# Performance work log

Measured on AMD Instinct MI355X. Metric: run time of the kernel, lower is better.

## Reference

```python
import jax, jax.numpy as jnp
import numpy as np

B, L = 1024, 64          # sentences, tokens per sentence
V, E = 100000, 300       # vocab, embedding dim
RH, M, NC = 50, 50, 3    # rnn_hidden, mem_dim, num_class
N = B * L                # total tree nodes


def setup_inputs() -> dict:
    key = jax.random.key(0)
    ks = jax.random.split(key, 24)
    rn = lambda k, s, sc=0.05: jax.random.normal(k, s, dtype=jnp.float32) * sc
    # balanced binary dependency tree per sentence: parent(i) = (i-1)//2
    loc = np.arange(L)
    par_loc = np.where(loc == 0, -1, (loc - 1) // 2)
    parent = np.where(par_loc[None, :] < 0, -1,
                      par_loc[None, :] + np.arange(B)[:, None] * L).reshape(-1)
    depth = np.tile(np.floor(np.log2(loc + 1)).astype(np.int64), B)
    tm = np.zeros(L, np.float32); tm[1:4] = 1.0  # 3 aspect-target tokens/sentence
    return {
        "embed_ids": jax.random.randint(ks[0], (B, L), 0, V),
        "parent": jnp.asarray(parent),
        "depth": jnp.asarray(depth),
        "target_mask": jnp.asarray(np.tile(tm, B)),
        "num_levels": 7,
        "embed_table": rn(ks[1], (V, E), 1.0),
        "W_ih_f": rn(ks[2], (4 * RH, E)), "W_hh_f": rn(ks[3], (4 * RH, RH)),
        "b_f": rn(ks[4], (4 * RH,)),
        "W_ih_b": rn(ks[5], (4 * RH, E)), "W_hh_b": rn(ks[6], (4 * RH, RH)),
        "b_b": rn(ks[7], (4 * RH,)),
        "W_iou": rn(ks[8], (3 * M, 2 * RH)),
        "U_iou_w": rn(ks[9], (3 * M, M)), "U_iou_b": rn(ks[10], (3 * M,)),
        "b_iou": jnp.zeros((3 * M,), jnp.float32),
        "U_f_w": rn(ks[11], (M, M)), "U_f_b": rn(ks[12], (M,)),
        "H_w": rn(ks[13], (M, 2 * RH)), "H_b": rn(ks[14], (M,)),
        "C_w": rn(ks[15], (NC, M)), "C_b": rn(ks[16], (NC,)),
    }


def _lstm(x, W_ih, W_hh, b, reverse):
    # x: (B, L, E) -> (B, L, H); PyTorch gate order i, f, g, o
    xg = jnp.einsum('ble,ge->blg', x, W_ih) + b
    H = W_hh.shape[1]
    def step(carry, xt):
        h, c = carry
        g = xt + h @ W_hh.T
        i, f, gg, o = jnp.split(g, 4, axis=-1)
        c = jax.nn.sigmoid(f) * c + jax.nn.sigmoid(i) * jnp.tanh(gg)
        h = jax.nn.sigmoid(o) * jnp.tanh(c)
        return (h, c), h
    z = jnp.zeros((x.shape[0], H), x.dtype)
    _, hs = jax.lax.scan(step, (z, z), jnp.swapaxes(xg, 0, 1), reverse=reverse)
    return jnp.swapaxes(hs, 0, 1)


def reference(embed_ids, parent, depth, target_mask, num_levels, embed_table,
              W_ih_f, W_hh_f, b_f, W_ih_b, W_hh_b, b_b,
              W_iou, U_iou_w, U_iou_b, b_iou, U_f_w, U_f_b,
              H_w, H_b, C_w, C_b):
    # --- BiLSTM encoder (dropout = identity at inference) ---
    emb = embed_table[embed_ids]                       # (B,L,E) gather
    hf = _lstm(emb, W_ih_f, W_hh_f, b_f, False)
    hb = _lstm(emb, W_ih_b, W_hh_b, b_b, True)
    x = jnp.concatenate([hf, hb], -1).reshape(N, 2 * RH)
    # --- ChildSum TreeLSTM, topological (deepest level first) ---
    iou0 = x @ W_iou.T                                 # (N, 3M)
    h_init = x @ H_w.T + H_b                           # (N, M)
    parent_safe = jnp.where(parent >= 0, parent, N)    # roots -> dummy slot N
    counts = jnp.zeros(N + 1, jnp.int32).at[parent_safe].add(1)
    has_children = (counts[:N] > 0)[:, None]
    h_fin = h_init
    c_fin = jnp.zeros((N, M), jnp.float32)
    h_sum = jnp.zeros((N + 1, M), jnp.float32)         # sum of child h
    fc_sum = jnp.zeros((N + 1, M), jnp.float32)        # sum of f * child c
    for lvl in range(num_levels - 1, -1, -1):
        m = (depth == lvl)[:, None]
        # reduce: leaves never get U_iou bias (no mailbox in DGL)
        iou = iou0 + jnp.where(has_children, h_sum[:N] @ U_iou_w.T + U_iou_b, 0.0) + b_iou
        i, o, u = jnp.split(iou, 3, axis=-1)
        c_new = jax.nn.sigmoid(i) * jnp.tanh(u) + fc_sum[:N]
        h_new = h_init + jax.nn.sigmoid(o) * jnp.tanh(c_new)
        h_fin = jnp.where(m, h_new, h_fin)
        c_fin = jnp.where(m, c_new, c_fin)
        # scatter messages from this level's nodes to their parents
        f = jax.nn.sigmoid(h_new @ U_f_w.T + U_f_b)
        h_sum = h_sum.at[parent_safe].add(jnp.where(m, h_new, 0.0))
        fc_sum = fc_sum.at[parent_safe].add(jnp.where(m, f * c_new, 0.0))
    # --- masked mean pool over target tokens per sentence ---
    tm = target_mask.reshape(B, L)
    pooled = (h_fin.reshape(B, L, M) * tm[:, :, None]).sum(1) / tm.sum(1, keepdims=True)
    logits = pooled @ C_w.T + C_b
    return logits, pooled
```

## Files before the change

### kernel.cpp

```cpp
#include <hip/hip_runtime.h>


typedef __attribute__((ext_vector_type(8))) short bf16x8;
typedef __attribute__((ext_vector_type(4))) float f32x4;

__device__ __forceinline__ float fsig2(float x) {
    float e = __builtin_amdgcn_exp2f(-1.4426950408889634f * x);
    return __builtin_amdgcn_rcpf(1.0f + e);
}
__device__ __forceinline__ float ftanh2(float x) {
    float e = __builtin_amdgcn_exp2f(2.8853900817779268f * x);
    return 1.0f - 2.0f * __builtin_amdgcn_rcpf(1.0f + e);
}

__device__ __forceinline__ unsigned short rne_bf16(float f) {
    unsigned u = __builtin_bit_cast(unsigned, f);
    unsigned r = u + 0x7fffu + ((u >> 16) & 1u);
    return (unsigned short)(r >> 16);
}
__device__ __forceinline__ void split2(float f, unsigned short& h, unsigned short& l) {
    h = rne_bf16(f);
    float fh = __builtin_bit_cast(float, ((unsigned)h) << 16);
    float r = f - fh;
    l = rne_bf16(r);
}

__device__ __forceinline__ void async_lds16(const void* g, void* l) {
    __builtin_amdgcn_global_load_lds(
        (const __attribute__((address_space(1))) unsigned int*)g,
        (__attribute__((address_space(3))) unsigned int*)l, 16, 0, 0);
}

__device__ __forceinline__ bf16x8 pack8(const unsigned short* h) {
    bf16x8 v;
    #pragma unroll
    for (int e = 0; e < 8; ++e) v[e] = (short)h[e];
    return v;
}

__device__ __forceinline__ void conv_item(int q, const float* __restrict__ B1,
                                          const float* __restrict__ B2,
                                          int split, int K, int Rreal, int BN,
                                          unsigned short* __restrict__ out) {
    int n  = q % BN;
    int kq = (q / BN) & 3;
    int c  = q / (BN * 4);
    const float* row = (n < split) ? (B1 + (size_t)n * K) : (B2 + (size_t)(n - split) * K);
    unsigned short h[8], l[8];
    #pragma unroll
    for (int e = 0; e < 8; ++e) {
        int k = c * 32 + kq * 8 + e;
        float v = (n < Rreal && k < K) ? row[k] : 0.0f;
        split2(v, h[e], l[e]);
    }
    size_t hb = ((((size_t)c * 2 + 0) * 4 + kq) * BN + n) * 8;
    size_t lb = ((((size_t)c * 2 + 1) * 4 + kq) * BN + n) * 8;
    *(ushort4*)&out[hb]     = make_ushort4(h[0], h[1], h[2], h[3]);
    *(ushort4*)&out[hb + 4] = make_ushort4(h[4], h[5], h[6], h[7]);
    *(ushort4*)&out[lb]     = make_ushort4(l[0], l[1], l[2], l[3]);
    *(ushort4*)&out[lb + 4] = make_ushort4(l[4], l[5], l[6], l[7]);
}

constexpr int WHC_DIR = 2 * 2 * 4 * 208 * 8;

__global__ void conv_fused(const float* __restrict__ Wihf, const float* __restrict__ Wihb,
                           const float* __restrict__ Wiou, const float* __restrict__ Hw,
                           const float* __restrict__ Whhf, const float* __restrict__ Whhb,
                           unsigned short* __restrict__ B1c,
                           unsigned short* __restrict__ B3c,
                           unsigned short* __restrict__ Whc) {
    int q = blockIdx.x * 256 + threadIdx.x;
    if (q < 17920) {
        conv_item(q, Wihf, Wihb, 200, 300, 400, 448, B1c);
    } else if (q < 22016) {
        conv_item(q - 17920, Wiou, Hw, 150, 100, 200, 256, B3c);
    } else if (q < 23680) {
        conv_item(q - 22016, Whhf, Whhf, 200, 50, 200, 208, Whc);
    } else if (q < 25344) {
        conv_item(q - 23680, Whhb, Whhb, 200, 50, 200, 208, Whc + WHC_DIR);
    }
}

template<int BN, int KCH, int KREAL, int NCOLS, bool GATHER>
__global__ __launch_bounds__(256)
void gemm_db(const float* __restrict__ A, const int* __restrict__ ids,
             const unsigned short* __restrict__ Bc,
             const float* __restrict__ bias1, const float* __restrict__ bias2,
             int split, float* __restrict__ C) {
    static_assert(KREAL % 8 == 4, "tail fixup assumes KREAL%8==4");
    static_assert(KCH % 2 == 0, "paired bodies");
    constexpr int NTW = BN / 64;
    constexpr int CHB = 64 * BN;
    constexpr int DMA_PT = BN / 32;
    __shared__ __align__(16) unsigned short As[2][2 * 4 * 64 * 8];
    __shared__ __align__(16) unsigned short Bt[2][CHB];

    const int tid = threadIdx.x;
    const int m0 = blockIdx.x * 64;
    const int w = tid >> 6, lane = tid & 63;
    const int r16 = lane & 15, quad = lane >> 4;
    const int wn = w * (BN / 4);

    const int mA = tid & 63, kqA = tid >> 6;
    const float* arow = GATHER ? (A + (size_t)ids[m0 + mA] * KREAL)
                               : (A + (size_t)(m0 + mA) * KREAL);

    auto stageB = [&](int c, int slot) {
        int cc = (c < KCH) ? c : (KCH - 1);
        const unsigned short* src = Bc + (size_t)cc * CHB + tid * 8;
        unsigned short* dst = &Bt[slot][tid * 8];
        #pragma unroll
        for (int i = 0; i < DMA_PT; ++i)
            async_lds16(src + (size_t)i * 2048, dst + i * 2048);
    };
    auto issueA = [&](int c, float4& p, float4& q) {
        int cc = (c < KCH) ? c : (KCH - 1);
        int k0 = cc * 32 + kqA * 8;
        const float* src = arow + ((k0 <= KREAL - 8) ? k0 : (KREAL - 8));
        p = *(const float4*)src;
        q = *(const float4*)(src + 4);
    };
    auto asWrite = [&](int c, float4 p, float4 q) {
        float ar[8];
        int k0 = c * 32 + kqA * 8;
        if (k0 <= KREAL - 8) {
            ar[0]=p.x; ar[1]=p.y; ar[2]=p.z; ar[3]=p.w;
            ar[4]=q.x; ar[5]=q.y; ar[6]=q.z; ar[7]=q.w;
        } else {
            ar[0] = (k0 + 0 < KREAL) ? q.x : 0.0f;
            ar[1] = (k0 + 1 < KREAL) ? q.y : 0.0f;
            ar[2] = (k0 + 2 < KREAL) ? q.z : 0.0f;
            ar[3] = (k0 + 3 < KREAL) ? q.w : 0.0f;
            ar[4] = 0.0f; ar[5] = 0.0f; ar[6] = 0.0f; ar[7] = 0.0f;
        }
        unsigned short h[8], l[8];
        #pragma unroll
        for (int e = 0; e < 8; ++e) split2(ar[e], h[e], l[e]);
        *(bf16x8*)&As[c & 1][((0 * 4 + kqA) * 64 + mA) * 8] = pack8(h);
        *(bf16x8*)&As[c & 1][((1 * 4 + kqA) * 64 + mA) * 8] = pack8(l);
    };

    f32x4 acc[4][NTW] = {};

    auto body = [&](int c, float4& wrP, float4& wrQ, float4& ldP, float4& ldQ) {
        stageB(c + 1, (c + 1) & 1);
        __builtin_amdgcn_sched_barrier(0);
        issueA(c + 2, ldP, ldQ);
        __builtin_amdgcn_sched_barrier(0);
        asWrite(c + 1, wrP, wrQ);
        bf16x8 af[2][4];
        #pragma unroll
        for (int i = 0; i < 4; ++i) {
            af[0][i] = *(const bf16x8*)&As[c & 1][((0 * 4 + quad) * 64 + i * 16 + r16) * 8];
            af[1][i] = *(const bf16x8*)&As[c & 1][((1 * 4 + quad) * 64 + i * 16 + r16) * 8];
        }
        #pragma unroll
        for (int t = 0; t < NTW; ++t) {
            bf16x8 bh = *(const bf16x8*)&Bt[c & 1][((0 * 4 + quad) * BN + wn + t * 16 + r16) * 8];
            bf16x8 bl = *(const bf16x8*)&Bt[c & 1][((1 * 4 + quad) * BN + wn + t * 16 + r16) * 8];
            #pragma unroll
            for (int i = 0; i < 4; ++i) {
                acc[i][t] = __builtin_amdgcn_mfma_f32_16x16x32_bf16(af[0][i], bh, acc[i][t], 0, 0, 0);
                acc[i][t] = __builtin_amdgcn_mfma_f32_16x16x32_bf16(af[1][i], bh, acc[i][t], 0, 0, 0);
                acc[i][t] = __builtin_amdgcn_mfma_f32_16x16x32_bf16(af[0][i], bl, acc[i][t], 0, 0, 0);
            }
        }
        asm volatile("s_waitcnt lgkmcnt(0) vmcnt(2)" ::: "memory");
        __builtin_amdgcn_sched_barrier(0);
        __builtin_amdgcn_s_barrier();
        __builtin_amdgcn_sched_barrier(0);
    };

    float4 pA, qA, pB, qB;
    stageB(0, 0);
    __builtin_amdgcn_sched_barrier(0);
    issueA(0, pA, qA);
    issueA(1, pB, qB);
    __syncthreads();
    asWrite(0, pA, qA);
    __syncthreads();

    #pragma unroll 1
    for (int c2 = 0; c2 < KCH / 2; ++c2) {
        body(2 * c2,     pB, qB, pA, qA);
        body(2 * c2 + 1, pA, qA, pB, qB);
    }

    #pragma unroll
    for (int t = 0; t < NTW; ++t) {
        int ncol = wn + t * 16 + r16;
        if (ncol < NCOLS) {
            float bv = (ncol < split) ? bias1[ncol] : bias2[ncol - split];
            #pragma unroll
            for (int i = 0; i < 4; ++i)
                #pragma unroll
                for (int r = 0; r < 4; ++r) {
                    int mrow = m0 + i * 16 + quad * 4 + r;
                    C[(size_t)mrow * NCOLS + ncol] = acc[i][t][r] + bv;
                }
        }
    }
}

__global__ __launch_bounds__(256)
void lstm_mfma(const float* __restrict__ xg, const unsigned short* __restrict__ Whc,
               float* __restrict__ x) {
    const int bi = blockIdx.x;
    const int dir = bi & 1;
    const int b0 = (bi >> 1) * 8;
    const int tid = threadIdx.x;
    const int w = tid >> 6, lane = tid & 63;
    const int r16 = lane & 15, quad = lane >> 4;

    __shared__ __align__(16) unsigned short Ah[8 * 16 * 8];
    __shared__ __align__(16) unsigned short Al[8 * 16 * 8];
    __shared__ __align__(16) float G[208 * 20];
    __shared__ __align__(16) float Xs[3][8][268];

    const int n0 = (w == 0) ? 0 : (w == 1) ? 4 : (w == 2) ? 7 : 10;
    const int nc = (w == 0) ? 4 : 3;

    const unsigned short* Wd = Whc + (size_t)dir * WHC_DIR;
    bf16x8 bfr[4][2][2];
    #pragma unroll
    for (int t = 0; t < 4; ++t) {
        int col = (n0 + ((t < nc) ? t : 0)) * 16 + r16;
        #pragma unroll
        for (int c = 0; c < 2; ++c)
            #pragma unroll
            for (int h = 0; h < 2; ++h)
                bfr[t][c][h] = *(const bf16x8*)&Wd[((((size_t)c * 2 + h) * 4 + quad) * 208 + col) * 8];
    }

    for (int q = tid; q < 512; q += 256) {
        ((unsigned*)Ah)[q] = 0u;
        ((unsigned*)Al)[q] = 0u;
    }

    int ss[2], ms[2];
    bool act[2];
    #pragma unroll
    for (int j = 0; j < 2; ++j) {
        int q = w * 100 + lane + 64 * j;
        ss[j] = q & 7;
        ms[j] = q >> 3;
        act[j] = (lane + 64 * j) < 100;
    }
    float c_reg[2] = {0.0f, 0.0f};

    #pragma unroll
    for (int p = 0; p < 2; ++p) {
        int idx0 = dir ? (63 - p) : p;
        #pragma unroll
        for (int i = 0; i < 2; ++i) {
            int s = w * 2 + i;
            const float* src = xg + ((size_t)(b0 + s) * 64 + idx0) * 400 + dir * 200 + lane * 4;
            async_lds16(src, &Xs[p][s][lane * 4]);
        }
    }
    __syncthreads();

    for (int step = 0; step < 64; ++step) {
        const int buf = step % 3;
        const int idx = dir ? (63 - step) : step;
        {
            int stepn = step + 2; if (stepn > 63) stepn = 63;
            const int slot = (step + 2) % 3;
            const int idxn = dir ? (63 - stepn) : stepn;
            #pragma unroll
            for (int i = 0; i < 2; ++i) {
                int s = w * 2 + i;
                const float* src = xg + ((size_t)(b0 + s) * 64 + idxn) * 400 + dir * 200 + lane * 4;
                async_lds16(src, &Xs[slot][s][lane * 4]);
            }
            __builtin_amdgcn_sched_barrier(0);
        }
        bf16x8 ah[2], al[2];
        #pragma unroll
        for (int c = 0; c < 2; ++c) {
            ah[c] = *(const bf16x8*)&Ah[((c * 4 + quad) * 16 + r16) * 8];
            al[c] = *(const bf16x8*)&Al[((c * 4 + quad) * 16 + r16) * 8];
        }
        f32x4 acc[4] = {};
        #pragma unroll
        for (int t = 0; t < 4; ++t) {
            if (t < nc) {
                #pragma unroll
                for (int c = 0; c < 2; ++c) {
                    acc[t] = __builtin_amdgcn_mfma_f32_16x16x32_bf16(ah[c], bfr[t][c][0], acc[t], 0, 0, 0);
                    acc[t] = __builtin_amdgcn_mfma_f32_16x16x32_bf16(al[c], bfr[t][c][0], acc[t], 0, 0, 0);
                    acc[t] = __builtin_amdgcn_mfma_f32_16x16x32_bf16(ah[c], bfr[t][c][1], acc[t], 0, 0, 0);
                }
            }
        }
        #pragma unroll
        for (int t = 0; t < 4; ++t) {
            if (t < nc) {
                int col = (n0 + t) * 16 + r16;
                *(f32x4*)&G[col * 20 + quad * 4] = acc[t];
            }
        }
        asm volatile("s_waitcnt lgkmcnt(0) vmcnt(8)" ::: "memory");
        __builtin_amdgcn_sched_barrier(0);
        __builtin_amdgcn_s_barrier();
        __builtin_amdgcn_sched_barrier(0);
        #pragma unroll
        for (int j = 0; j < 2; ++j) {
            if (act[j]) {
                int s = ss[j], m = ms[j];
                float gi = G[m * 20 + s]         + Xs[buf][s][m];
                float gf = G[(m + 50) * 20 + s]  + Xs[buf][s][m + 50];
                float gg = G[(m + 100) * 20 + s] + Xs[buf][s][m + 100];
                float go = G[(m + 150) * 20 + s] + Xs[buf][s][m + 150];
                c_reg[j] = fsig2(gf) * c_reg[j] + fsig2(gi) * ftanh2(gg);
                float h = fsig2(go) * ftanh2(c_reg[j]);
                unsigned short hh, hl;
                split2(h, hh, hl);
                Ah[(m >> 3) * 128 + s * 8 + (m & 7)] = hh;
                Al[(m >> 3) * 128 + s * 8 + (m & 7)] = hl;
                x[((size_t)(b0 + s) * 64 + idx) * 100 + dir * 50 + m] = h;
            }
        }
        asm volatile("s_waitcnt lgkmcnt(0)" ::: "memory");
        __builtin_amdgcn_sched_barrier(0);
        __builtin_amdgcn_s_barrier();
        __builtin_amdgcn_sched_barrier(0);
    }
}

__global__ __launch_bounds__(256)
void tree_kernel(const float* __restrict__ C2,
                 const float* __restrict__ Uw, const float* __restrict__ Ub,
                 const float* __restrict__ Fw, const float* __restrict__ Fb,
                 const float* __restrict__ tmask,
                 const float* __restrict__ Cw, const float* __restrict__ Cb,
                 float* __restrict__ out) {
    const int tid = threadIdx.x;
    const int w = tid >> 6, lane = tid & 63;
    const int s = blockIdx.x * 4 + w;

    __shared__ __align__(16) float Us[150][52];
    __shared__ __align__(16) float Fs[50][52];
    __shared__ __align__(16) float HS[4][32][52];
    __shared__ __align__(16) float FC[4][32][52];
    __shared__ __align__(16) float HV[4][64];
    __shared__ __align__(16) float TMS[4][64];

    for (int q = tid; q < 7500; q += 256) Us[q / 50][q % 50] = Uw[q];
    for (int q = tid; q < 2500; q += 256) Fs[q / 50][q % 50] = Fw[q];
    for (int q = tid; q < 4 * 32 * 52; q += 256) {
        int ww = q / (32 * 52), r = q - ww * (32 * 52);
        HS[ww][r / 52][r % 52] = 0.0f;
        FC[ww][r / 52][r % 52] = 0.0f;
    }
    TMS[w][lane] = tmask[(size_t)s * 64 + lane];
    __syncthreads();

    const bool act = lane < 50;
    const int m = act ? lane : 49;
    const float ub0 = Ub[m], ub1 = Ub[50 + m], ub2 = Ub[100 + m];
    const float fb = Fb[m];
    const float* c2s = C2 + (size_t)s * 64 * 200;

    float pr = 0.0f;
    float pc0, pc1, pc2, pc3;
    {
        const float* nb = c2s + 63 * 200;
        pc0 = nb[m]; pc1 = nb[50 + m]; pc2 = nb[100 + m]; pc3 = nb[150 + m];
    }

    for (int l = 6; l >= 0; --l) {
        const int lo = (1 << l) - 1;
        const int hi = min((1 << (l + 1)) - 2, 63);
        for (int loc = lo; loc <= hi; ++loc) {
            const int nxt = (loc < hi) ? (loc + 1) : ((l > 0) ? ((1 << (l - 1)) - 1) : loc);
            float nc0, nc1, nc2, nc3;
            {
                const float* nb = c2s + (size_t)nxt * 200;
                nc0 = nb[m]; nc1 = nb[50 + m]; nc2 = nb[100 + m]; nc3 = nb[150 + m];
            }
            const bool hasch = (loc <= 31);
            float mi = 0.0f, mo = 0.0f, mu = 0.0f, fcv = 0.0f;
            if (hasch) {
                const float* hs = &HS[w][loc][0];
                const float* u0 = &Us[m][0];
                const float* u1 = &Us[50 + m][0];
                const float* u2 = &Us[100 + m][0];
                float i0=0,i1=0,i2=0,i3=0, o0=0,o1=0,o2=0,o3=0, g0=0,g1=0,g2=0,g3=0;
                #pragma unroll
                for (int j = 0; j < 12; ++j) {
                    float4 h4 = *(const float4*)&hs[j * 4];
                    float4 a4 = *(const float4*)&u0[j * 4];
                    float4 b4 = *(const float4*)&u1[j * 4];
                    float4 c4 = *(const float4*)&u2[j * 4];
                    i0 += a4.x*h4.x; i1 += a4.y*h4.y; i2 += a4.z*h4.z; i3 += a4.w*h4.w;
                    o0 += b4.x*h4.x; o1 += b4.y*h4.y; o2 += b4.z*h4.z; o3 += b4.w*h4.w;
                    g0 += c4.x*h4.x; g1 += c4.y*h4.y; g2 += c4.z*h4.z; g3 += c4.w*h4.w;
                }
                float h48 = hs[48], h49 = hs[49];
                mi = ub0 + (i0 + i1) + (i2 + i3) + u0[48]*h48 + u0[49]*h49;
                mo = ub1 + (o0 + o1) + (o2 + o3) + u1[48]*h48 + u1[49]*h49;
                mu = ub2 + (g0 + g1) + (g2 + g3) + u2[48]*h48 + u2[49]*h49;
                fcv = FC[w][loc][m];
            }
            float ig = pc0 + mi, og = pc1 + mo, ug = pc2 + mu;
            float cn = fsig2(ig) * ftanh2(ug) + fcv;
            float hn = pc3 + fsig2(og) * ftanh2(cn);
            pr += TMS[w][loc] * hn;
            if (act) HV[w][lane] = hn;
            {
                const float* hv = &HV[w][0];
                const float* f0 = &Fs[m][0];
                float a0 = 0, a1 = 0, a2 = 0, a3 = 0;
                #pragma unroll
                for (int j = 0; j < 12; ++j) {
                    float4 h4 = *(const float4*)&hv[j * 4];
                    float4 f4 = *(const float4*)&f0[j * 4];
                    a0 += f4.x*h4.x; a1 += f4.y*h4.y; a2 += f4.z*h4.z; a3 += f4.w*h4.w;
                }
                float facc = fb + (a0 + a1) + (a2 + a3) + f0[48]*hv[48] + f0[49]*hv[49];
                if (act && loc > 0) {
                    int p = (loc - 1) >> 1;
                    float fm = fsig2(facc) * cn;
                    HS[w][p][lane] += hn;
                    FC[w][p][lane] += fm;
                }
            }
            pc0 = nc0; pc1 = nc1; pc2 = nc2; pc3 = nc3;
        }
    }

    float ws = 0.0f;
    #pragma unroll
    for (int j = 0; j < 16; ++j) {
        float4 t4 = *(const float4*)&TMS[w][j * 4];
        ws += (t4.x + t4.y) + (t4.z + t4.w);
    }
    float p = pr / ws;
    if (act) {
        out[3072 + (size_t)s * 50 + lane] = p;
        HV[w][lane] = p;
    }
    if (lane < 3) {
        float acc = Cb[lane];
        const float* crow = Cw + lane * 50;
        for (int k = 0; k < 50; ++k) acc += crow[k] * HV[w][k];
        out[(size_t)s * 3 + lane] = acc;
    }
}

extern "C" void kernel_launch(void* const* d_in, const int* in_sizes, int n_in,
                              void* d_out, int out_size, void* d_ws, size_t ws_size,
                              hipStream_t stream) {
    (void)in_sizes; (void)n_in; (void)out_size; (void)ws_size;
    const int*   ids   = (const int*)d_in[0];
    const float* tmask = (const float*)d_in[3];
    const float* table = (const float*)d_in[5];
    const float* Wihf  = (const float*)d_in[6];
    const float* Whhf  = (const float*)d_in[7];
    const float* bf    = (const float*)d_in[8];
    const float* Wihb  = (const float*)d_in[9];
    const float* Whhb  = (const float*)d_in[10];
    const float* bb    = (const float*)d_in[11];
    const float* Wiou  = (const float*)d_in[12];
    const float* Uiouw = (const float*)d_in[13];
    const float* Uioub = (const float*)d_in[14];
    const float* biou  = (const float*)d_in[15];
    const float* Ufw   = (const float*)d_in[16];
    const float* Ufb   = (const float*)d_in[17];
    const float* Hw    = (const float*)d_in[18];
    const float* Hb    = (const float*)d_in[19];
    const float* Cw    = (const float*)d_in[20];
    const float* Cb    = (const float*)d_in[21];
    float* out = (float*)d_out;

    float* wsf = (float*)d_ws;
    float* xg = wsf;
    float* x  = wsf + (size_t)65536 * 400;
    float* C2 = wsf;
    unsigned short* B1c = (unsigned short*)(wsf + 32768000);
    unsigned short* B3c = (unsigned short*)(wsf + 32911360);
    unsigned short* Whc = (unsigned short*)(wsf + 32944128);

    conv_fused<<<99, 256, 0, stream>>>(Wihf, Wihb, Wiou, Hw, Whhf, Whhb,
                                       B1c, B3c, Whc);
    gemm_db<448, 10, 300, 400, true><<<1024, 256, 0, stream>>>(
        table, ids, B1c, bf, bb, 200, xg);
    lstm_mfma<<<256, 256, 0, stream>>>(xg, Whc, x);
    gemm_db<256, 4, 100, 200, false><<<1024, 256, 0, stream>>>(
        x, nullptr, B3c, biou, Hb, 150, C2);
    tree_kernel<<<256, 256, 0, stream>>>(
        C2, Uiouw, Uioub, Ufw, Ufb, tmask, Cw, Cb, out);
}
```

Baseline: 462.2 us.

## Single-buffer B tile in LDS by hoisting B fragments into registers

The GEMM kernel now keeps a single LDS buffer for the B tile instead of two. It first loads all B fragments for the chunk into registers, then synchronizes and issues the async load of the next chunk into the same buffer. Launch bounds ask for two blocks per CU. The aim is to halve B's LDS footprint so occupancy can rise, at the cost of more registers and an extra barrier per iteration, which exposes the B load latency before the MFMAs.

```diff
diff --git a/kernel.cpp b/kernel.cpp
--- a/kernel.cpp
+++ b/kernel.cpp
@@ -82,18 +82,18 @@
 }
 
 template<int BN, int KCH, int KREAL, int NCOLS, bool GATHER>
-__global__ __launch_bounds__(256)
-void gemm_db(const float* __restrict__ A, const int* __restrict__ ids,
-             const unsigned short* __restrict__ Bc,
-             const float* __restrict__ bias1, const float* __restrict__ bias2,
-             int split, float* __restrict__ C) {
+__global__ __launch_bounds__(256, 2)
+void gemm_hoist(const float* __restrict__ A, const int* __restrict__ ids,
+                const unsigned short* __restrict__ Bc,
+                const float* __restrict__ bias1, const float* __restrict__ bias2,
+                int split, float* __restrict__ C) {
     static_assert(KREAL % 8 == 4, "tail fixup assumes KREAL%8==4");
     static_assert(KCH % 2 == 0, "paired bodies");
     constexpr int NTW = BN / 64;
     constexpr int CHB = 64 * BN;
     constexpr int DMA_PT = BN / 32;
     __shared__ __align__(16) unsigned short As[2][2 * 4 * 64 * 8];
-    __shared__ __align__(16) unsigned short Bt[2][CHB];
+    __shared__ __align__(16) unsigned short Bt[CHB];
 
     const int tid = threadIdx.x;
     const int m0 = blockIdx.x * 64;
@@ -105,10 +105,10 @@
     const float* arow = GATHER ? (A + (size_t)ids[m0 + mA] * KREAL)
                                : (A + (size_t)(m0 + mA) * KREAL);
 
-    auto stageB = [&](int c, int slot) {
+    auto stageB = [&](int c) {
         int cc = (c < KCH) ? c : (KCH - 1);
         const unsigned short* src = Bc + (size_t)cc * CHB + tid * 8;
-        unsigned short* dst = &Bt[slot][tid * 8];
+        unsigned short* dst = &Bt[tid * 8];
         #pragma unroll
         for (int i = 0; i < DMA_PT; ++i)
             async_lds16(src + (size_t)i * 2048, dst + i * 2048);
@@ -143,7 +143,17 @@
     f32x4 acc[4][NTW] = {};
 
     auto body = [&](int c, float4& wrP, float4& wrQ, float4& ldP, float4& ldQ) {
-        stageB(c + 1, (c + 1) & 1);
+        bf16x8 bh[NTW], bl[NTW];
+        #pragma unroll
+        for (int t = 0; t < NTW; ++t) {
+            bh[t] = *(const bf16x8*)&Bt[((0 * 4 + quad) * BN + wn + t * 16 + r16) * 8];
+            bl[t] = *(const bf16x8*)&Bt[((1 * 4 + quad) * BN + wn + t * 16 + r16) * 8];
+        }
+        asm volatile("s_waitcnt lgkmcnt(0)" ::: "memory");
+        __builtin_amdgcn_sched_barrier(0);
+        __builtin_amdgcn_s_barrier();
+        __builtin_amdgcn_sched_barrier(0);
+        stageB(c + 1);
         __builtin_amdgcn_sched_barrier(0);
         issueA(c + 2, ldP, ldQ);
         __builtin_amdgcn_sched_barrier(0);
@@ -156,13 +166,11 @@
         }
         #pragma unroll
         for (int t = 0; t < NTW; ++t) {
-            bf16x8 bh = *(const bf16x8*)&Bt[c & 1][((0 * 4 + quad) * BN + wn + t * 16 + r16) * 8];
-            bf16x8 bl = *(const bf16x8*)&Bt[c & 1][((1 * 4 + quad) * BN + wn + t * 16 + r16) * 8];
             #pragma unroll
             for (int i = 0; i < 4; ++i) {
-                acc[i][t] = __builtin_amdgcn_mfma_f32_16x16x32_bf16(af[0][i], bh, acc[i][t], 0, 0, 0);
-                acc[i][t] = __builtin_amdgcn_mfma_f32_16x16x32_bf16(af[1][i], bh, acc[i][t], 0, 0, 0);
-                acc[i][t] = __builtin_amdgcn_mfma_f32_16x16x32_bf16(af[0][i], bl, acc[i][t], 0, 0, 0);
+                acc[i][t] = __builtin_amdgcn_mfma_f32_16x16x32_bf16(af[0][i], bh[t], acc[i][t], 0, 0, 0);
+                acc[i][t] = __builtin_amdgcn_mfma_f32_16x16x32_bf16(af[1][i], bh[t], acc[i][t], 0, 0, 0);
+                acc[i][t] = __builtin_amdgcn_mfma_f32_16x16x32_bf16(af[0][i], bl[t], acc[i][t], 0, 0, 0);
             }
         }
         asm volatile("s_waitcnt lgkmcnt(0) vmcnt(2)" ::: "memory");
@@ -172,7 +180,7 @@
     };
 
     float4 pA, qA, pB, qB;
-    stageB(0, 0);
+    stageB(0);
     __builtin_amdgcn_sched_barrier(0);
     issueA(0, pA, qA);
     issueA(1, pB, qB);
@@ -484,10 +492,10 @@
 
     conv_fused<<<99, 256, 0, stream>>>(Wihf, Wihb, Wiou, Hw, Whhf, Whhb,
                                        B1c, B3c, Whc);
-    gemm_db<448, 10, 300, 400, true><<<1024, 256, 0, stream>>>(
+    gemm_hoist<448, 10, 300, 400, true><<<1024, 256, 0, stream>>>(
         table, ids, B1c, bf, bb, 200, xg);
     lstm_mfma<<<256, 256, 0, stream>>>(xg, Whc, x);
-    gemm_db<256, 4, 100, 200, false><<<1024, 256, 0, stream>>>(
+    gemm_hoist<256, 4, 100, 200, false><<<1024, 256, 0, stream>>>(
         x, nullptr, B3c, biou, Hb, 150, C2);
     tree_kernel<<<256, 256, 0, stream>>>(
         C2, Uiouw, Uioub, Ufw, Ufb, tmask, Cw, Cb, out);
```

Result: faster. 421.8 us (-8.7%).
